# Optimization experiments

Measured on AMD Instinct MI355X. Metric: run time of the kernel, lower is better.

The kernel has to match this reference:

```python
import jax, jax.numpy as jnp
import numpy as np

N_NODES = 100000
N_EDGES = 3200000
N_GRAPHS = 128
HID = 64


def gcn_conv(x, src, dst, W, b, n_nodes):
    # PyG GCNConv: add self-loops, symmetric normalization, scatter-add aggregate
    loop = jnp.arange(n_nodes, dtype=src.dtype)
    s = jnp.concatenate([src, loop])
    d = jnp.concatenate([dst, loop])
    deg = jax.ops.segment_sum(jnp.ones_like(d, dtype=x.dtype), d, num_segments=n_nodes)
    dinv = jnp.where(deg > 0, jax.lax.rsqrt(deg), 0.0)
    norm = dinv[s] * dinv[d]                      # [E+N]
    h = x @ W                                     # [N, out] small GEMM first
    msg = h[s] * norm[:, None]                    # [E+N, out] gather + scale
    out = jax.ops.segment_sum(msg, d, num_segments=n_nodes)
    return out + b


def setup_inputs() -> dict:
    key = jax.random.key(0)
    ks = jax.random.split(key, 9)
    x = jax.random.normal(ks[0], (N_NODES, 2), dtype=jnp.float32)
    edge_index = jax.random.randint(ks[1], (2, N_EDGES), 0, N_NODES, dtype=jnp.int64 if jax.config.jax_enable_x64 else jnp.int32)
    batch = jnp.sort(jax.random.randint(ks[2], (N_NODES,), 0, N_GRAPHS, dtype=edge_index.dtype))
    W1 = jax.random.normal(ks[3], (2, HID), dtype=jnp.float32) / jnp.sqrt(2.0)
    b1 = jax.random.normal(ks[4], (HID,), dtype=jnp.float32) * 0.01
    W2 = jax.random.normal(ks[5], (HID, HID), dtype=jnp.float32) / jnp.sqrt(float(HID))
    b2 = jax.random.normal(ks[6], (HID,), dtype=jnp.float32) * 0.01
    Wfc = jax.random.normal(ks[7], (HID, 1), dtype=jnp.float32) / jnp.sqrt(float(HID))
    bfc = jax.random.normal(ks[8], (1,), dtype=jnp.float32) * 0.01
    return {"x": x, "edge_index": edge_index, "batch": batch,
            "W1": W1, "b1": b1, "W2": W2, "b2": b2, "Wfc": Wfc, "bfc": bfc}


def reference(x, edge_index, batch, W1, b1, W2, b2, Wfc, bfc):
    src, dst = edge_index[0], edge_index[1]
    h = jax.nn.relu(gcn_conv(x, src, dst, W1, b1, N_NODES))
    h = jax.nn.relu(gcn_conv(h, src, dst, W2, b2, N_NODES))
    # global mean pool over graphs
    sums = jax.ops.segment_sum(h, batch, num_segments=N_GRAPHS)
    cnts = jax.ops.segment_sum(jnp.ones((N_NODES,), dtype=h.dtype), batch, num_segments=N_GRAPHS)
    pooled = sums / jnp.maximum(cnts, 1.0)[:, None]   # [G, HID]
    return pooled @ Wfc + bfc                          # [G, 1]
```

## Files before the change

kernel.cpp:

```cpp
#include <hip/hip_runtime.h>

constexpr int N  = 100000;
constexpr int E  = 3200000;
constexpr int G  = 128;
constexpr int H  = 64;

__device__ __forceinline__ unsigned short f32_to_bf16_rne(float x) {
    unsigned int u = __float_as_uint(x);
    unsigned int r = (u + 0x7FFFu + ((u >> 16) & 1u)) >> 16;
    return (unsigned short)r;
}
__device__ __forceinline__ float bflo(unsigned int u) { return __uint_as_float(u << 16); }
__device__ __forceinline__ float bfhi(unsigned int u) { return __uint_as_float(u & 0xFFFF0000u); }

__global__ __launch_bounds__(256) void k_count(const int* __restrict__ dst,
                                               int* __restrict__ cnt) {
    int e = blockIdx.x * 256 + threadIdx.x;
    if (e < E) atomicAdd(&cnt[dst[e]], 1);
}

__global__ __launch_bounds__(256) void k_dinv(const float* __restrict__ x,
                                              const int* __restrict__ cnt,
                                              float* __restrict__ dinv,
                                              float2* __restrict__ gx) {
    int v = blockIdx.x * 256 + threadIdx.x;
    if (v < N) {
        float d = rsqrtf((float)(cnt[v] + 1));
        dinv[v] = d;
        float2 xv = ((const float2*)x)[v];
        gx[v] = make_float2(xv.x * d, xv.y * d);
    }
}

__global__ __launch_bounds__(1024) void k_scan(const int* __restrict__ cnt,
                                               int* __restrict__ offs,
                                               int* __restrict__ cursor) {
    constexpr int T = 1024;
    constexpr int PER = (N + T - 1) / T;
    int tid = threadIdx.x;
    int begin = tid * PER;
    int end = begin + PER; if (end > N) end = N;

    int total = 0;
    for (int i = begin; i < end; ++i) total += cnt[i];

    __shared__ int wsum[16];
    int lane = tid & 63, wid = tid >> 6;
    int incl = total;
    #pragma unroll
    for (int off = 1; off < 64; off <<= 1) {
        int t = __shfl_up(incl, off);
        if (lane >= off) incl += t;
    }
    if (lane == 63) wsum[wid] = incl;
    __syncthreads();
    if (wid == 0 && lane < 16) {
        int w = wsum[lane];
        #pragma unroll
        for (int off = 1; off < 16; off <<= 1) {
            int t = __shfl_up(w, off);
            if (lane >= off) w += t;
        }
        wsum[lane] = w;
    }
    __syncthreads();
    int waveBase = (wid == 0) ? 0 : wsum[wid - 1];
    int run = waveBase + (incl - total);
    for (int i = begin; i < end; ++i) {
        offs[i] = run;
        cursor[i] = run;
        run += cnt[i];
    }
}

__global__ __launch_bounds__(256) void k_fill(const int* __restrict__ src,
                                              const int* __restrict__ dst,
                                              int* __restrict__ cursor,
                                              int* __restrict__ csr) {
    int e = blockIdx.x * 256 + threadIdx.x;
    if (e < E) {
        int d = dst[e];
        int pos = atomicAdd(&cursor[d], 1);
        csr[pos] = src[e];
    }
}

__global__ __launch_bounds__(256) void k_agg1(const int* __restrict__ csr,
                                              const int* __restrict__ offs,
                                              const int* __restrict__ cnt,
                                              const float* __restrict__ dinv,
                                              const float2* __restrict__ gx,
                                              float2* __restrict__ aggx) {
    int lane = threadIdx.x & 63;
    int v = (blockIdx.x * 256 + threadIdx.x) >> 6;
    if (v >= N) return;
    int start = offs[v], dg = cnt[v];
    float ax = 0.f, ay = 0.f;
    for (int i = lane; i < dg; i += 64) {
        int s = csr[start + i];
        float2 g = gx[s];
        ax += g.x; ay += g.y;
    }
    #pragma unroll
    for (int off = 1; off < 64; off <<= 1) {
        ax += __shfl_xor(ax, off);
        ay += __shfl_xor(ay, off);
    }
    if (lane == 0) {
        float d = dinv[v];
        float2 g = gx[v];
        aggx[v] = make_float2(d * (ax + g.x), d * (ay + g.y));
    }
}

__global__ __launch_bounds__(256) void k_mlp(const float2* __restrict__ aggx,
                                             const float* __restrict__ W1,
                                             const float* __restrict__ b1,
                                             const float* __restrict__ W2,
                                             const float* __restrict__ dinv,
                                             unsigned short* __restrict__ g2b) {
    int lane = threadIdx.x & 63;
    int wave = (blockIdx.x * 256 + threadIdx.x) >> 6;
    int nw = gridDim.x * 4;

    float w2col[64];
    #pragma unroll
    for (int k = 0; k < 64; ++k) w2col[k] = W2[k * 64 + lane];
    float w10 = W1[lane], w11 = W1[64 + lane], bb = b1[lane];

    for (int v = wave; v < N; v += nw) {
        float2 a = aggx[v];
        float tt = fmaxf(fmaf(a.y, w11, fmaf(a.x, w10, bb)), 0.f);
        float a0 = 0.f, a1 = 0.f, a2 = 0.f, a3 = 0.f;
        #pragma unroll
        for (int k = 0; k < 64; k += 4) {
            float t0 = __int_as_float(__builtin_amdgcn_readlane(__float_as_int(tt), k + 0));
            float t1 = __int_as_float(__builtin_amdgcn_readlane(__float_as_int(tt), k + 1));
            float t2 = __int_as_float(__builtin_amdgcn_readlane(__float_as_int(tt), k + 2));
            float t3 = __int_as_float(__builtin_amdgcn_readlane(__float_as_int(tt), k + 3));
            a0 = fmaf(t0, w2col[k + 0], a0);
            a1 = fmaf(t1, w2col[k + 1], a1);
            a2 = fmaf(t2, w2col[k + 2], a2);
            a3 = fmaf(t3, w2col[k + 3], a3);
        }
        float val = ((a0 + a1) + (a2 + a3)) * dinv[v];
        g2b[(size_t)v * 64 + lane] = f32_to_bf16_rne(val);
    }
}

__global__ __launch_bounds__(256) void k_agg2(const int* __restrict__ csr,
                                              const int* __restrict__ offs,
                                              const int* __restrict__ cnt,
                                              const float* __restrict__ dinv,
                                              const float* __restrict__ b2,
                                              const unsigned short* __restrict__ g2b,
                                              const int* __restrict__ batch,
                                              float* __restrict__ pooled,
                                              int* __restrict__ cntg) {
    int lane = threadIdx.x & 63;
    int v = (blockIdx.x * 256 + threadIdx.x) >> 6;
    if (v >= N) return;
    int half = lane >> 5;
    int c = lane & 31;
    int start = offs[v], dg = cnt[v];
    const unsigned int* g2u = (const unsigned int*)g2b;

    float aLo = 0.f, aHi = 0.f;

    int base = 0;
    while (base < dg) {
        int chunk = dg - base; if (chunk > 64) chunk = 64;
        int idx = csr[start + base + lane];
        int npair = (chunk + 1) >> 1;
        for (int p0 = 0; p0 < npair; p0 += 8) {
            unsigned int u[8];
            int okm[8];
            #pragma unroll
            for (int k = 0; k < 8; ++k) {
                int p = p0 + k;
                int e = (p << 1) | half;
                bool ok = (p < npair) && (e < chunk);
                okm[k] = ok ? -1 : 0;
                int jA = p << 1;       if (jA > chunk - 1) jA = chunk - 1;
                int jB = (p << 1) | 1; if (jB > chunk - 1) jB = chunk - 1;
                int rA = __builtin_amdgcn_readlane(idx, jA);
                int rB = __builtin_amdgcn_readlane(idx, jB);
                int row = half ? rB : rA;
                u[k] = g2u[((size_t)row << 5) + c];
            }
            #pragma unroll
            for (int k = 0; k < 8; ++k) {
                unsigned int uu = u[k] & (unsigned int)okm[k];
                aLo += bflo(uu);
                aHi += bfhi(uu);
            }
        }
        base += chunk;
    }

    aLo += __shfl_xor(aLo, 32);
    aHi += __shfl_xor(aHi, 32);

    if (half == 0) {
        unsigned int s = g2u[((size_t)v << 5) + c];
        aLo += bflo(s);
        aHi += bfhi(s);
        float d = dinv[v];
        int c0 = c << 1;
        float o0 = fmaxf(fmaf(d, aLo, b2[c0 + 0]), 0.f);
        float o1 = fmaxf(fmaf(d, aHi, b2[c0 + 1]), 0.f);
        int b = batch[v];
        atomicAdd(&pooled[b * 64 + c0 + 0], o0);
        atomicAdd(&pooled[b * 64 + c0 + 1], o1);
        if (lane == 0) atomicAdd(&cntg[b], 1);
    }
}

__global__ __launch_bounds__(64) void k_final(const float* __restrict__ pooled,
                                              const int* __restrict__ cntg,
                                              const float* __restrict__ Wfc,
                                              const float* __restrict__ bfc,
                                              float* __restrict__ out) {
    int g = blockIdx.x;
    int j = threadIdx.x;
    float c = fmaxf((float)cntg[g], 1.f);
    float p = (pooled[g * 64 + j] / c) * Wfc[j];
    #pragma unroll
    for (int off = 32; off >= 1; off >>= 1) p += __shfl_down(p, off);
    if (j == 0) out[g] = p + bfc[0];
}

extern "C" void kernel_launch(void* const* d_in, const int* in_sizes, int n_in,
                              void* d_out, int out_size, void* d_ws, size_t ws_size,
                              hipStream_t stream) {
    const float* x     = (const float*)d_in[0];
    const int*   edge  = (const int*)d_in[1];
    const int*   batch = (const int*)d_in[2];
    const float* W1    = (const float*)d_in[3];
    const float* b1    = (const float*)d_in[4];
    const float* W2    = (const float*)d_in[5];
    const float* b2    = (const float*)d_in[6];
    const float* Wfc   = (const float*)d_in[7];
    const float* bfc   = (const float*)d_in[8];
    float* out = (float*)d_out;

    const int* src = edge;
    const int* dst = edge + E;

    char* base = (char*)d_ws;
    size_t o = 0;
    auto alloc = [&](size_t bytes) -> void* {
        void* p = base + o;
        o += (bytes + 1023) & ~size_t(1023);
        return p;
    };
    int*    cnt    = (int*)alloc((size_t)N * 4);
    float*  dinv   = (float*)alloc((size_t)N * 4);
    float2* gx     = (float2*)alloc((size_t)N * 8);
    float2* aggx   = (float2*)alloc((size_t)N * 8);
    int*    offs   = (int*)alloc((size_t)N * 4);
    int*    cursor = (int*)alloc((size_t)N * 4);
    int*    csr    = (int*)alloc((size_t)E * 4 + 1024);
    unsigned short* g2b = (unsigned short*)alloc((size_t)N * H * 2);
    float*  pooled = (float*)alloc((size_t)G * H * 4);
    int*    cntg   = (int*)alloc((size_t)G * 4);

    hipMemsetAsync(cnt, 0, (size_t)N * 4, stream);
    hipMemsetAsync(pooled, 0, (size_t)G * H * 4, stream);
    hipMemsetAsync(cntg, 0, (size_t)G * 4, stream);

    k_count<<<(E + 255) / 256, 256, 0, stream>>>(dst, cnt);
    k_dinv<<<(N + 255) / 256, 256, 0, stream>>>(x, cnt, dinv, gx);
    k_scan<<<1, 1024, 0, stream>>>(cnt, offs, cursor);
    k_fill<<<(E + 255) / 256, 256, 0, stream>>>(src, dst, cursor, csr);
    k_agg1<<<(N + 3) / 4, 256, 0, stream>>>(csr, offs, cnt, dinv, gx, aggx);
    k_mlp<<<1024, 256, 0, stream>>>(aggx, W1, b1, W2, dinv, g2b);
    k_agg2<<<(N + 3) / 4, 256, 0, stream>>>(csr, offs, cnt, dinv, b2, g2b, batch, pooled, cntg);
    k_final<<<G, 64, 0, stream>>>(pooled, cntg, Wfc, bfc, out);
}
```

Measured before the change: 1.342 ms.

## Partition CSR by source tile and run second aggregation per tile

Edges are bucketed by source-node range into four tiles, giving four CSR segments per destination. This needs a four-way count, a multi-block scan and four fill passes. The second aggregation then runs one pass per tile, accumulating partial sums in an fp32 buffer, so each pass gathers from only a quarter of the bf16 feature table and that slice can stay cache-resident. The cost is extra launches, four passes over the edge list during fill, and read-modify-write traffic on a 25.6 MB accumulator.

Measured after the change: 1.084 ms. -19.3%, faster.

```diff
diff --git a/kernel.cpp b/kernel.cpp
--- a/kernel.cpp
+++ b/kernel.cpp
@@ -4,6 +4,10 @@
 constexpr int E  = 3200000;
 constexpr int G  = 128;
 constexpr int H  = 64;
+constexpr int NT   = 4;
+constexpr int TILE = 25000;
+constexpr int M4   = NT * N;
+constexpr int NB   = (M4 + 1023) / 1024;
 
 __device__ __forceinline__ unsigned short f32_to_bf16_rne(float x) {
     unsigned int u = __float_as_uint(x);
@@ -13,93 +17,131 @@
 __device__ __forceinline__ float bflo(unsigned int u) { return __uint_as_float(u << 16); }
 __device__ __forceinline__ float bfhi(unsigned int u) { return __uint_as_float(u & 0xFFFF0000u); }
 
-__global__ __launch_bounds__(256) void k_count(const int* __restrict__ dst,
-                                               int* __restrict__ cnt) {
+__global__ __launch_bounds__(256) void k_count4(const int* __restrict__ src,
+                                                const int* __restrict__ dst,
+                                                int* __restrict__ cnt4) {
     int e = blockIdx.x * 256 + threadIdx.x;
-    if (e < E) atomicAdd(&cnt[dst[e]], 1);
+    if (e < E) {
+        int t = src[e] / TILE;
+        atomicAdd(&cnt4[t * N + dst[e]], 1);
+    }
 }
 
 __global__ __launch_bounds__(256) void k_dinv(const float* __restrict__ x,
-                                              const int* __restrict__ cnt,
+                                              const int* __restrict__ cnt4,
                                               float* __restrict__ dinv,
                                               float2* __restrict__ gx) {
     int v = blockIdx.x * 256 + threadIdx.x;
     if (v < N) {
-        float d = rsqrtf((float)(cnt[v] + 1));
+        int deg = cnt4[v] + cnt4[N + v] + cnt4[2 * N + v] + cnt4[3 * N + v] + 1;
+        float d = rsqrtf((float)deg);
         dinv[v] = d;
         float2 xv = ((const float2*)x)[v];
         gx[v] = make_float2(xv.x * d, xv.y * d);
     }
 }
 
-__global__ __launch_bounds__(1024) void k_scan(const int* __restrict__ cnt,
-                                               int* __restrict__ offs,
-                                               int* __restrict__ cursor) {
-    constexpr int T = 1024;
-    constexpr int PER = (N + T - 1) / T;
-    int tid = threadIdx.x;
-    int begin = tid * PER;
-    int end = begin + PER; if (end > N) end = N;
-
-    int total = 0;
-    for (int i = begin; i < end; ++i) total += cnt[i];
-
-    __shared__ int wsum[16];
-    int lane = tid & 63, wid = tid >> 6;
-    int incl = total;
+__global__ __launch_bounds__(1024) void k_scan1(const int* __restrict__ cnt4,
+                                                int* __restrict__ offs4,
+                                                int* __restrict__ blksum) {
+    int i = blockIdx.x * 1024 + threadIdx.x;
+    int v = (i < M4) ? cnt4[i] : 0;
+    int lane = threadIdx.x & 63, wid = threadIdx.x >> 6;
+    int incl = v;
     #pragma unroll
     for (int off = 1; off < 64; off <<= 1) {
         int t = __shfl_up(incl, off);
         if (lane >= off) incl += t;
     }
-    if (lane == 63) wsum[wid] = incl;
+    __shared__ int ws[16];
+    if (lane == 63) ws[wid] = incl;
     __syncthreads();
     if (wid == 0 && lane < 16) {
-        int w = wsum[lane];
+        int w = ws[lane];
         #pragma unroll
         for (int off = 1; off < 16; off <<= 1) {
             int t = __shfl_up(w, off);
             if (lane >= off) w += t;
         }
-        wsum[lane] = w;
+        ws[lane] = w;
     }
     __syncthreads();
-    int waveBase = (wid == 0) ? 0 : wsum[wid - 1];
-    int run = waveBase + (incl - total);
-    for (int i = begin; i < end; ++i) {
-        offs[i] = run;
-        cursor[i] = run;
-        run += cnt[i];
-    }
-}
-
-__global__ __launch_bounds__(256) void k_fill(const int* __restrict__ src,
-                                              const int* __restrict__ dst,
-                                              int* __restrict__ cursor,
-                                              int* __restrict__ csr) {
+    int base = (wid == 0) ? 0 : ws[wid - 1];
+    if (i < M4) offs4[i] = base + incl - v;
+    if (threadIdx.x == 0) blksum[blockIdx.x] = ws[15];
+}
+
+__global__ __launch_bounds__(512) void k_scan2(int* __restrict__ blksum) {
+    int i = threadIdx.x;
+    int v = (i < NB) ? blksum[i] : 0;
+    int lane = i & 63, wid = i >> 6;
+    int incl = v;
+    #pragma unroll
+    for (int off = 1; off < 64; off <<= 1) {
+        int t = __shfl_up(incl, off);
+        if (lane >= off) incl += t;
+    }
+    __shared__ int ws[8];
+    if (lane == 63) ws[wid] = incl;
+    __syncthreads();
+    if (wid == 0 && lane < 8) {
+        int w = ws[lane];
+        #pragma unroll
+        for (int off = 1; off < 8; off <<= 1) {
+            int t = __shfl_up(w, off);
+            if (lane >= off) w += t;
+        }
+        ws[lane] = w;
+    }
+    __syncthreads();
+    int base = (wid == 0) ? 0 : ws[wid - 1];
+    if (i < NB) blksum[i] = base + incl - v;
+}
+
+__global__ __launch_bounds__(1024) void k_scan3(int* __restrict__ offs4,
+                                                int* __restrict__ cursor4,
+                                                const int* __restrict__ blksum) {
+    int i = blockIdx.x * 1024 + threadIdx.x;
+    if (i < M4) {
+        int o = offs4[i] + blksum[blockIdx.x];
+        offs4[i] = o;
+        cursor4[i] = o;
+    }
+}
+
+__global__ __launch_bounds__(256) void k_fill4(const int* __restrict__ src,
+                                               const int* __restrict__ dst,
+                                               int* __restrict__ cursor4,
+                                               int* __restrict__ csr,
+                                               int t) {
     int e = blockIdx.x * 256 + threadIdx.x;
     if (e < E) {
-        int d = dst[e];
-        int pos = atomicAdd(&cursor[d], 1);
-        csr[pos] = src[e];
+        int s = src[e];
+        if (s / TILE == t) {
+            int pos = atomicAdd(&cursor4[t * N + dst[e]], 1);
+            csr[pos] = s;
+        }
     }
 }
 
 __global__ __launch_bounds__(256) void k_agg1(const int* __restrict__ csr,
-                                              const int* __restrict__ offs,
-                                              const int* __restrict__ cnt,
+                                              const int* __restrict__ offs4,
+                                              const int* __restrict__ cnt4,
                                               const float* __restrict__ dinv,
                                               const float2* __restrict__ gx,
                                               float2* __restrict__ aggx) {
     int lane = threadIdx.x & 63;
     int v = (blockIdx.x * 256 + threadIdx.x) >> 6;
     if (v >= N) return;
-    int start = offs[v], dg = cnt[v];
     float ax = 0.f, ay = 0.f;
-    for (int i = lane; i < dg; i += 64) {
-        int s = csr[start + i];
-        float2 g = gx[s];
-        ax += g.x; ay += g.y;
+    #pragma unroll
+    for (int t = 0; t < NT; ++t) {
+        int st = offs4[t * N + v], len = cnt4[t * N + v];
+        for (int i = lane; i < len; i += 64) {
+            int s = csr[st + i];
+            float2 g = gx[s];
+            ax += g.x; ay += g.y;
+        }
     }
     #pragma unroll
     for (int off = 1; off < 64; off <<= 1) {
@@ -148,21 +190,24 @@
     }
 }
 
-__global__ __launch_bounds__(256) void k_agg2(const int* __restrict__ csr,
-                                              const int* __restrict__ offs,
-                                              const int* __restrict__ cnt,
-                                              const float* __restrict__ dinv,
-                                              const float* __restrict__ b2,
-                                              const unsigned short* __restrict__ g2b,
-                                              const int* __restrict__ batch,
-                                              float* __restrict__ pooled,
-                                              int* __restrict__ cntg) {
+template<int MODE>
+__global__ __launch_bounds__(256) void k_agg2t(const int* __restrict__ csr,
+                                               const int* __restrict__ offs4,
+                                               const int* __restrict__ cnt4,
+                                               const float* __restrict__ dinv,
+                                               const float* __restrict__ b2,
+                                               const unsigned short* __restrict__ g2b,
+                                               const int* __restrict__ batch,
+                                               float2* __restrict__ acc2,
+                                               float* __restrict__ pooled,
+                                               int* __restrict__ cntg,
+                                               int t) {
     int lane = threadIdx.x & 63;
     int v = (blockIdx.x * 256 + threadIdx.x) >> 6;
     if (v >= N) return;
     int half = lane >> 5;
     int c = lane & 31;
-    int start = offs[v], dg = cnt[v];
+    int st = offs4[t * N + v], dg = cnt4[t * N + v];
     const unsigned int* g2u = (const unsigned int*)g2b;
 
     float aLo = 0.f, aHi = 0.f;
@@ -170,7 +215,7 @@
     int base = 0;
     while (base < dg) {
         int chunk = dg - base; if (chunk > 64) chunk = 64;
-        int idx = csr[start + base + lane];
+        int idx = csr[st + base + lane];
         int npair = (chunk + 1) >> 1;
         for (int p0 = 0; p0 < npair; p0 += 8) {
             unsigned int u[8];
@@ -202,17 +247,26 @@
     aHi += __shfl_xor(aHi, 32);
 
     if (half == 0) {
-        unsigned int s = g2u[((size_t)v << 5) + c];
-        aLo += bflo(s);
-        aHi += bfhi(s);
-        float d = dinv[v];
-        int c0 = c << 1;
-        float o0 = fmaxf(fmaf(d, aLo, b2[c0 + 0]), 0.f);
-        float o1 = fmaxf(fmaf(d, aHi, b2[c0 + 1]), 0.f);
-        int b = batch[v];
-        atomicAdd(&pooled[b * 64 + c0 + 0], o0);
-        atomicAdd(&pooled[b * 64 + c0 + 1], o1);
-        if (lane == 0) atomicAdd(&cntg[b], 1);
+        size_t ai = (size_t)v * 32 + c;
+        if (MODE == 0) {
+            acc2[ai] = make_float2(aLo, aHi);
+        } else if (MODE == 1) {
+            float2 p = acc2[ai];
+            acc2[ai] = make_float2(p.x + aLo, p.y + aHi);
+        } else {
+            float2 p = acc2[ai];
+            unsigned int s = g2u[((size_t)v << 5) + c];
+            float sLo = p.x + aLo + bflo(s);
+            float sHi = p.y + aHi + bfhi(s);
+            float d = dinv[v];
+            int c0 = c << 1;
+            float o0 = fmaxf(fmaf(d, sLo, b2[c0 + 0]), 0.f);
+            float o1 = fmaxf(fmaf(d, sHi, b2[c0 + 1]), 0.f);
+            int b = batch[v];
+            atomicAdd(&pooled[b * 64 + c0 + 0], o0);
+            atomicAdd(&pooled[b * 64 + c0 + 1], o1);
+            if (lane == 0) atomicAdd(&cntg[b], 1);
+        }
     }
 }
 
@@ -254,27 +308,39 @@
         o += (bytes + 1023) & ~size_t(1023);
         return p;
     };
-    int*    cnt    = (int*)alloc((size_t)N * 4);
-    float*  dinv   = (float*)alloc((size_t)N * 4);
-    float2* gx     = (float2*)alloc((size_t)N * 8);
-    float2* aggx   = (float2*)alloc((size_t)N * 8);
-    int*    offs   = (int*)alloc((size_t)N * 4);
-    int*    cursor = (int*)alloc((size_t)N * 4);
-    int*    csr    = (int*)alloc((size_t)E * 4 + 1024);
+    int*    cnt4    = (int*)alloc((size_t)M4 * 4);
+    int*    offs4   = (int*)alloc((size_t)M4 * 4);
+    int*    cursor4 = (int*)alloc((size_t)M4 * 4);
+    int*    blksum  = (int*)alloc((size_t)NB * 4);
+    float*  dinv    = (float*)alloc((size_t)N * 4);
+    float2* gx      = (float2*)alloc((size_t)N * 8);
+    float2* aggx    = (float2*)alloc((size_t)N * 8);
+    int*    csr     = (int*)alloc((size_t)E * 4 + 1024);
     unsigned short* g2b = (unsigned short*)alloc((size_t)N * H * 2);
-    float*  pooled = (float*)alloc((size_t)G * H * 4);
-    int*    cntg   = (int*)alloc((size_t)G * 4);
-
-    hipMemsetAsync(cnt, 0, (size_t)N * 4, stream);
+    float2* acc2    = (float2*)alloc((size_t)N * 32 * 8);
+    float*  pooled  = (float*)alloc((size_t)G * H * 4);
+    int*    cntg    = (int*)alloc((size_t)G * 4);
+
+    hipMemsetAsync(cnt4, 0, (size_t)M4 * 4, stream);
     hipMemsetAsync(pooled, 0, (size_t)G * H * 4, stream);
     hipMemsetAsync(cntg, 0, (size_t)G * 4, stream);
 
-    k_count<<<(E + 255) / 256, 256, 0, stream>>>(dst, cnt);
-    k_dinv<<<(N + 255) / 256, 256, 0, stream>>>(x, cnt, dinv, gx);
-    k_scan<<<1, 1024, 0, stream>>>(cnt, offs, cursor);
-    k_fill<<<(E + 255) / 256, 256, 0, stream>>>(src, dst, cursor, csr);
-    k_agg1<<<(N + 3) / 4, 256, 0, stream>>>(csr, offs, cnt, dinv, gx, aggx);
+    k_count4<<<(E + 255) / 256, 256, 0, stream>>>(src, dst, cnt4);
+    k_dinv<<<(N + 255) / 256, 256, 0, stream>>>(x, cnt4, dinv, gx);
+    k_scan1<<<NB, 1024, 0, stream>>>(cnt4, offs4, blksum);
+    k_scan2<<<1, 512, 0, stream>>>(blksum);
+    k_scan3<<<NB, 1024, 0, stream>>>(offs4, cursor4, blksum);
+    for (int t = 0; t < NT; ++t)
+        k_fill4<<<(E + 255) / 256, 256, 0, stream>>>(src, dst, cursor4, csr, t);
+    k_agg1<<<(N + 3) / 4, 256, 0, stream>>>(csr, offs4, cnt4, dinv, gx, aggx);
     k_mlp<<<1024, 256, 0, stream>>>(aggx, W1, b1, W2, dinv, g2b);
-    k_agg2<<<(N + 3) / 4, 256, 0, stream>>>(csr, offs, cnt, dinv, b2, g2b, batch, pooled, cntg);
+    k_agg2t<0><<<(N + 3) / 4, 256, 0, stream>>>(csr, offs4, cnt4, dinv, b2, g2b,
+                                                batch, acc2, pooled, cntg, 0);
+    k_agg2t<1><<<(N + 3) / 4, 256, 0, stream>>>(csr, offs4, cnt4, dinv, b2, g2b,
+                                                batch, acc2, pooled, cntg, 1);
+    k_agg2t<1><<<(N + 3) / 4, 256, 0, stream>>>(csr, offs4, cnt4, dinv, b2, g2b,
+                                                batch, acc2, pooled, cntg, 2);
+    k_agg2t<2><<<(N + 3) / 4, 256, 0, stream>>>(csr, offs4, cnt4, dinv, b2, g2b,
+                                                batch, acc2, pooled, cntg, 3);
     k_final<<<G, 64, 0, stream>>>(pooled, cntg, Wfc, bfc, out);
 }
```
